# Performance work log

Measured on AMD Instinct MI355X. Metric: run time of the kernel, lower is better.

Reference implementation:

```python
import jax, jax.numpy as jnp
import numpy as np

L, N, E, H = 4096, 1, 1024, 16
DH = E // H
SCALE = DH ** -0.5


def setup_inputs() -> dict:
    key = jax.random.key(0)
    k1, k2, k3 = jax.random.split(key, 3)
    # xavier_uniform-ish scales for faithfulness of magnitude
    lim_qkv = (6.0 / (3 * E + E)) ** 0.5
    lim_out = (6.0 / (E + E)) ** 0.5
    x = jax.random.normal(k1, (L, N, E), dtype=jnp.float32)
    w_qkv = jax.random.uniform(k2, (3 * E, E), dtype=jnp.float32, minval=-lim_qkv, maxval=lim_qkv)
    w_out = jax.random.uniform(k3, (E, E), dtype=jnp.float32, minval=-lim_out, maxval=lim_out)
    return {"x": x, "w_qkv": w_qkv, "w_out": w_out}


def reference(x, w_qkv, w_out):
    # x: [L, N, E]
    qkv = jnp.einsum('lne,fe->lnf', x, w_qkv)          # [L, N, 3E]
    q, k, v = jnp.split(qkv, 3, axis=-1)               # each [L, N, E]

    def to_heads(t):
        # [L, N, E] -> [N*H, L, DH]
        return t.reshape(L, N * H, DH).transpose(1, 0, 2)

    q = to_heads(q) * SCALE
    k = to_heads(k)
    v = to_heads(v)
    attn = jnp.einsum('bld,bmd->blm', q, k)            # [N*H, L, L]
    attn = jax.nn.softmax(attn, axis=-1)
    out = jnp.einsum('blm,bmd->bld', attn, v)          # [N*H, L, DH]
    out = out.transpose(1, 0, 2).reshape(L, N, E)
    return jnp.einsum('lne,fe->lnf', out, w_out)       # [L, N, E]
```

## Files before the change

### kernel.cpp

```cpp
#include <hip/hip_runtime.h>
#include <hip/hip_bf16.h>
#include <stdint.h>

#define L_SEQ 4096
#define EMB   1024
#define NHEAD 16
#define DHEAD 64

#define SM_SCALE 0.18033688011112042f
#define SM_FIXED_MAX 12.0f

typedef __attribute__((ext_vector_type(8))) short short8;
typedef __attribute__((ext_vector_type(4))) short s16x4;
typedef __attribute__((ext_vector_type(4))) float f32x4;
typedef __attribute__((ext_vector_type(2))) unsigned uint2v;

struct Pack8 { f32x4 lo, hi; };

__device__ inline short f2bf(float f) {
  union { float f; unsigned u; } c; c.f = f;
  unsigned r = (c.u + 0x7fffu + ((c.u >> 16) & 1u)) >> 16;
  return (short)(unsigned short)r;
}
__device__ inline unsigned fbits(float f) {
  union { float f; unsigned u; } c; c.f = f; return c.u;
}
__device__ inline unsigned pack_trunc(float f0, float f1) {
#if __has_builtin(__builtin_amdgcn_perm)
  return __builtin_amdgcn_perm(fbits(f1), fbits(f0), 0x07060302u);
#else
  return (fbits(f0) >> 16) | (fbits(f1) & 0xffff0000u);
#endif
}

#if __has_builtin(__builtin_amdgcn_exp2f)
#define EXP2F(x) __builtin_amdgcn_exp2f(x)
#else
#define EXP2F(x) exp2f(x)
#endif

__device__ inline void pl16swap(unsigned &x, unsigned &y) {
#if __has_builtin(__builtin_amdgcn_permlane16_swap)
  auto r = __builtin_amdgcn_permlane16_swap(x, y, false, false);
  x = r[0]; y = r[1];
#else
  asm volatile("v_permlane16_swap_b32 %0, %1" : "+v"(x), "+v"(y));
#endif
}

__device__ inline short8 mk8(unsigned d0, unsigned d1, unsigned d2, unsigned d3) {
  union { unsigned u[4]; short8 s; } c;
  c.u[0] = d0; c.u[1] = d1; c.u[2] = d2; c.u[3] = d3;
  return c.s;
}

template<bool F32>
__device__ inline auto ld8(const void* p, size_t off) {
  if constexpr (F32) {
    const float* f = (const float*)p + off;
    Pack8 r; r.lo = *(const f32x4*)f; r.hi = *(const f32x4*)(f + 4);
    return r;
  } else {
    return *(const short8*)((const short*)p + off);
  }
}
__device__ inline short8 cvt8(Pack8 r) {
  short8 o;
#pragma unroll
  for (int j = 0; j < 4; ++j) { o[j] = f2bf(r.lo[j]); o[4 + j] = f2bf(r.hi[j]); }
  return o;
}
__device__ inline short8 cvt8(short8 r) { return r; }

#define MFMA16(a, b, c) __builtin_amdgcn_mfma_f32_16x16x32_bf16(a, b, c, 0, 0, 0)
#define FZERO ((f32x4){0.f, 0.f, 0.f, 0.f})

__global__ __launch_bounds__(256)
void conv_kernel(const float* __restrict__ in, short* __restrict__ out, int n) {
  int i = (blockIdx.x * 256 + threadIdx.x) * 8;
  if (i >= n) return;
  Pack8 r; r.lo = *(const f32x4*)(in + i); r.hi = *(const f32x4*)(in + i + 4);
  *(short8*)(out + i) = cvt8(r);
}

template<bool AF32, bool BF32, bool CF32>
__global__ __launch_bounds__(256, 2)
void gemm_bt(const void* __restrict__ Av, const void* __restrict__ Bv,
             void* __restrict__ Cv, int N, int K, int lda, int ldc,
             float cscale) {
  __shared__ __align__(16) short At[128 * 40];
  __shared__ __align__(16) short Bt[128 * 40];

  const int tid  = threadIdx.x;
  const int lane = tid & 63;
  const int wave = tid >> 6;
  const int quad = lane >> 4;
  const int l15  = lane & 15;
  const int q8   = quad << 3;

  const int nbn = N >> 7;
  const int bm  = (blockIdx.x / nbn) << 7;
  const int bn  = (blockIdx.x % nbn) << 7;
  const int wr  = wave >> 1;
  const int wc  = wave & 1;

  const int s0 = tid, s1 = tid + 256;
  const int ar0 = s0 >> 2, ac0 = (s0 & 3) << 3;
  const int ar1 = s1 >> 2, ac1 = (s1 & 3) << 3;

  const size_t aoff0 = (size_t)(bm + ar0) * lda + ac0;
  const size_t aoff1 = (size_t)(bm + ar1) * lda + ac1;
  const size_t boff0 = (size_t)(bn + ar0) * K + ac0;
  const size_t boff1 = (size_t)(bn + ar1) * K + ac1;

  f32x4 acc[4][4];
#pragma unroll
  for (int r = 0; r < 4; ++r)
#pragma unroll
    for (int c = 0; c < 4; ++c) acc[r][c] = FZERO;

  auto ga0 = ld8<AF32>(Av, aoff0);
  auto ga1 = ld8<AF32>(Av, aoff1);
  auto gb0 = ld8<BF32>(Bv, boff0);
  auto gb1 = ld8<BF32>(Bv, boff1);

  const int arow = (wr * 64 + l15) * 40 + q8;
  const int brow = (wc * 64 + l15) * 40 + q8;

  const int nk = K >> 5;
  for (int kt = 0; kt < nk; ++kt) {
    __syncthreads();
    *(short8*)(At + ar0 * 40 + ac0) = cvt8(ga0);
    *(short8*)(At + ar1 * 40 + ac1) = cvt8(ga1);
    *(short8*)(Bt + ar0 * 40 + ac0) = cvt8(gb0);
    *(short8*)(Bt + ar1 * 40 + ac1) = cvt8(gb1);
    __syncthreads();

    if (kt + 1 < nk) {
      const size_t k0 = (size_t)(kt + 1) << 5;
      ga0 = ld8<AF32>(Av, aoff0 + k0);
      ga1 = ld8<AF32>(Av, aoff1 + k0);
      gb0 = ld8<BF32>(Bv, boff0 + k0);
      gb1 = ld8<BF32>(Bv, boff1 + k0);
    }

    short8 af[4], bf[4];
#pragma unroll
    for (int r = 0; r < 4; ++r) af[r] = *(const short8*)(At + arow + r * 640);
#pragma unroll
    for (int c = 0; c < 4; ++c) bf[c] = *(const short8*)(Bt + brow + c * 640);
#pragma unroll
    for (int r = 0; r < 4; ++r)
#pragma unroll
      for (int c = 0; c < 4; ++c)
        acc[r][c] = MFMA16(af[r], bf[c], acc[r][c]);
  }

#pragma unroll
  for (int r = 0; r < 4; ++r) {
#pragma unroll
    for (int c = 0; c < 4; ++c) {
      const int col = bn + wc * 64 + c * 16 + l15;
#pragma unroll
      for (int reg = 0; reg < 4; ++reg) {
        const int row = bm + wr * 64 + r * 16 + quad * 4 + reg;
        const float v = acc[r][c][reg] * cscale;
        if constexpr (CF32) ((float*)Cv)[(size_t)row * ldc + col] = v;
        else                ((short*)Cv)[(size_t)row * ldc + col] = f2bf(v);
      }
    }
  }
}

__global__ __launch_bounds__(256, 2)
void gemm_qkv(const short* __restrict__ A, const float* __restrict__ B,
              short* __restrict__ qb, short* __restrict__ kb,
              short* __restrict__ vt) {
  __shared__ __align__(16) short At[128 * 40];
  __shared__ __align__(16) short Bt[128 * 40];

  const int tid  = threadIdx.x;
  const int lane = tid & 63;
  const int wave = tid >> 6;
  const int quad = lane >> 4;
  const int l15  = lane & 15;
  const int q8   = quad << 3;

  const int bm  = (blockIdx.x / 24) << 7;
  const int bn  = (blockIdx.x % 24) << 7;
  const int wr  = wave >> 1;
  const int wc  = wave & 1;

  const int s0 = tid, s1 = tid + 256;
  const int ar0 = s0 >> 2, ac0 = (s0 & 3) << 3;
  const int ar1 = s1 >> 2, ac1 = (s1 & 3) << 3;

  const size_t aoff0 = (size_t)(bm + ar0) * EMB + ac0;
  const size_t aoff1 = (size_t)(bm + ar1) * EMB + ac1;
  const size_t boff0 = (size_t)(bn + ar0) * EMB + ac0;
  const size_t boff1 = (size_t)(bn + ar1) * EMB + ac1;

  f32x4 acc[4][4];
#pragma unroll
  for (int r = 0; r < 4; ++r)
#pragma unroll
    for (int c = 0; c < 4; ++c) acc[r][c] = FZERO;

  short8 ga0 = *(const short8*)(A + aoff0);
  short8 ga1 = *(const short8*)(A + aoff1);
  Pack8  gb0 = ld8<true>(B, boff0);
  Pack8  gb1 = ld8<true>(B, boff1);

  const int arow = (wr * 64 + l15) * 40 + q8;
  const int brow = (wc * 64 + l15) * 40 + q8;

  for (int kt = 0; kt < 32; ++kt) {
    __syncthreads();
    *(short8*)(At + ar0 * 40 + ac0) = ga0;
    *(short8*)(At + ar1 * 40 + ac1) = ga1;
    *(short8*)(Bt + ar0 * 40 + ac0) = cvt8(gb0);
    *(short8*)(Bt + ar1 * 40 + ac1) = cvt8(gb1);
    __syncthreads();

    if (kt + 1 < 32) {
      const size_t k0 = (size_t)(kt + 1) << 5;
      ga0 = *(const short8*)(A + aoff0 + k0);
      ga1 = *(const short8*)(A + aoff1 + k0);
      gb0 = ld8<true>(B, boff0 + k0);
      gb1 = ld8<true>(B, boff1 + k0);
    }

    short8 af[4], bf[4];
#pragma unroll
    for (int r = 0; r < 4; ++r) af[r] = *(const short8*)(At + arow + r * 640);
#pragma unroll
    for (int c = 0; c < 4; ++c) bf[c] = *(const short8*)(Bt + brow + c * 640);
#pragma unroll
    for (int r = 0; r < 4; ++r)
#pragma unroll
      for (int c = 0; c < 4; ++c)
        acc[r][c] = MFMA16(af[r], bf[c], acc[r][c]);
  }

  if (bn < 2048) {
    short* dst = (bn < 1024) ? qb : kb;
    const int bcol = (bn < 1024) ? bn : bn - 1024;
    const float cs = (bn < 1024) ? SM_SCALE : 1.0f;
#pragma unroll
    for (int r = 0; r < 4; ++r)
#pragma unroll
      for (int c = 0; c < 4; ++c) {
        const int col = bcol + wc * 64 + c * 16 + l15;
#pragma unroll
        for (int reg = 0; reg < 4; ++reg) {
          const int row = bm + wr * 64 + r * 16 + quad * 4 + reg;
          dst[(size_t)row * EMB + col] = f2bf(acc[r][c][reg] * cs);
        }
      }
  } else {
    const int bcol = bn - 2048;
#pragma unroll
    for (int r = 0; r < 4; ++r)
#pragma unroll
      for (int c = 0; c < 4; ++c) {
        const int col  = bcol + wc * 64 + c * 16 + l15;
        const int rowb = bm + wr * 64 + r * 16 + quad * 4;
        s16x4 pk;
#pragma unroll
        for (int reg = 0; reg < 4; ++reg) pk[reg] = f2bf(acc[r][c][reg]);
        *(s16x4*)(vt + (size_t)col * L_SEQ + rowb) = pk;
      }
  }
}

__global__ __launch_bounds__(256, 2)
void attn_kernel(short* __restrict__ qo, const short* __restrict__ kbuf,
                 const short* __restrict__ vtbuf) {
  __shared__ __align__(16) short Kt[2][64 * 72];
  __shared__ __align__(16) short Vt[2][64 * 72];

  const int tid  = threadIdx.x;
  const int lane = tid & 63;
  const int w    = tid >> 6;
  const int quad = lane >> 4;
  const int l15  = lane & 15;
  const int q8   = quad << 3;
  const int vb   = ((quad & 1) << 4) | ((quad >> 1) << 3);

  const int h    = blockIdx.x >> 5;
  const int qblk = blockIdx.x & 31;
  const int hcol = h * 64;

  const int srow = tid >> 3;
  const int sc8  = (tid & 7) << 3;

  short8 qf[2][2];
#pragma unroll
  for (int g = 0; g < 2; ++g) {
    const short* qp = qo + (size_t)(qblk * 128 + w * 32 + g * 16 + l15) * EMB + hcol;
    qf[g][0] = *(const short8*)(qp + q8);
    qf[g][1] = *(const short8*)(qp + 32 + q8);
  }

  const short8 vone = {0x3F80, 0x3F80, 0x3F80, 0x3F80,
                       0x3F80, 0x3F80, 0x3F80, 0x3F80};

  f32x4 o[2][4];
#pragma unroll
  for (int g = 0; g < 2; ++g)
#pragma unroll
    for (int f = 0; f < 4; ++f) o[g][f] = FZERO;
  f32x4 l_c[2] = {FZERO, FZERO};

  const size_t koff0 = (size_t)srow * EMB + hcol + sc8;
  const size_t voff0 = (size_t)(hcol + srow) * L_SEQ + sc8;
  const size_t krr = (size_t)32 * EMB;
  const size_t vrr = (size_t)32 * L_SEQ;

  short8 gk0 = *(const short8*)(kbuf + koff0);
  short8 gk1 = *(const short8*)(kbuf + koff0 + krr);
  short8 gv0 = *(const short8*)(vtbuf + voff0);
  short8 gv1 = *(const short8*)(vtbuf + voff0 + vrr);

  for (int t = 0; t < 64; ++t) {
    short* const ktb = &Kt[t & 1][0];
    short* const vtb = &Vt[t & 1][0];

    *(short8*)(ktb + srow * 72 + sc8) = gk0;
    *(short8*)(ktb + (srow + 32) * 72 + sc8) = gk1;
    *(short8*)(vtb + srow * 72 + sc8) = gv0;
    *(short8*)(vtb + (srow + 32) * 72 + sc8) = gv1;
    __syncthreads();

    if (t < 63) {
      const size_t kk = (size_t)(t + 1) * 64;
      gk0 = *(const short8*)(kbuf + koff0 + kk * EMB);
      gk1 = *(const short8*)(kbuf + koff0 + krr + kk * EMB);
      gv0 = *(const short8*)(vtbuf + voff0 + kk);
      gv1 = *(const short8*)(vtbuf + voff0 + vrr + kk);
    }

    f32x4 s[2][4];
#pragma unroll
    for (int f = 0; f < 4; ++f) {
      const int krow = (f * 16 + l15) * 72;
      short8 kf0 = *(const short8*)(ktb + krow + q8);
      short8 kf1 = *(const short8*)(ktb + krow + 32 + q8);
      s[0][f] = MFMA16(kf0, qf[0][0], FZERO);
      s[0][f] = MFMA16(kf1, qf[0][1], s[0][f]);
      s[1][f] = MFMA16(kf0, qf[1][0], FZERO);
      s[1][f] = MFMA16(kf1, qf[1][1], s[1][f]);
    }

    short8 pa[2][2];
#pragma unroll
    for (int g = 0; g < 2; ++g) {
      float p[4][4];
#pragma unroll
      for (int f = 0; f < 4; ++f)
#pragma unroll
        for (int r = 0; r < 4; ++r)
          p[f][r] = EXP2F(s[g][f][r] - SM_FIXED_MAX);

      unsigned pk[4][2];
#pragma unroll
      for (int f = 0; f < 4; ++f) {
        pk[f][0] = pack_trunc(p[f][0], p[f][1]);
        pk[f][1] = pack_trunc(p[f][2], p[f][3]);
      }
      pl16swap(pk[0][0], pk[1][0]);
      pl16swap(pk[0][1], pk[1][1]);
      pl16swap(pk[2][0], pk[3][0]);
      pl16swap(pk[2][1], pk[3][1]);
      pa[g][0] = mk8(pk[0][0], pk[0][1], pk[1][0], pk[1][1]);
      pa[g][1] = mk8(pk[2][0], pk[2][1], pk[3][0], pk[3][1]);

      f32x4 rsv = MFMA16(pa[g][0], vone, FZERO);
      rsv = MFMA16(pa[g][1], vone, rsv);
#pragma unroll
      for (int r = 0; r < 4; ++r) l_c[g][r] += rsv[r];
    }

#pragma unroll
    for (int f = 0; f < 4; ++f) {
      const int vrow = (f * 16 + l15) * 72;
      short8 v0 = *(const short8*)(vtb + vrow + vb);
      short8 v1 = *(const short8*)(vtb + vrow + 32 + vb);
      o[0][f] = MFMA16(pa[0][0], v0, o[0][f]);
      o[0][f] = MFMA16(pa[0][1], v1, o[0][f]);
      o[1][f] = MFMA16(pa[1][0], v0, o[1][f]);
      o[1][f] = MFMA16(pa[1][1], v1, o[1][f]);
    }
  }

  __syncthreads();
  short* const pw = &Kt[0][0] + w * (32 * 72);
#pragma unroll
  for (int g = 0; g < 2; ++g) {
    f32x4 inv;
#pragma unroll
    for (int r = 0; r < 4; ++r) inv[r] = 1.0f / l_c[g][r];
    short* const pg = pw + g * (16 * 72);
#pragma unroll
    for (int f = 0; f < 4; ++f)
#pragma unroll
      for (int r = 0; r < 4; ++r)
        pg[(quad * 4 + r) * 72 + f * 16 + l15] = f2bf(o[g][f][r] * inv[r]);
  }

#pragma unroll
  for (int rr = 0; rr < 4; ++rr) {
    const int row = (lane >> 3) + rr * 8;
    const int c8  = (lane & 7) << 3;
    short8 gv = *(const short8*)(pw + row * 72 + c8);
    *(short8*)(qo + (size_t)(qblk * 128 + w * 32 + row) * EMB + hcol + c8) = gv;
  }
}

extern "C" void kernel_launch(void* const* d_in, const int* in_sizes, int n_in,
                              void* d_out, int out_size, void* d_ws, size_t ws_size,
                              hipStream_t stream) {
  (void)in_sizes; (void)n_in; (void)out_size; (void)ws_size;
  const float* x     = (const float*)d_in[0];
  const float* w_qkv = (const float*)d_in[1];
  const float* w_out = (const float*)d_in[2];

  short* qbuf  = (short*)d_ws;
  short* x_bf  = qbuf + (size_t)L_SEQ * EMB;
  short* wo_bf = x_bf;
  short* kbuf  = (short*)d_out;
  short* vtbuf = kbuf + (size_t)L_SEQ * EMB;
  float* outp  = (float*)d_out;

  conv_kernel<<<dim3(L_SEQ * EMB / 2048), 256, 0, stream>>>(x, x_bf, L_SEQ * EMB);

  gemm_qkv<<<dim3(768), 256, 0, stream>>>(x_bf, w_qkv, qbuf, kbuf, vtbuf);

  conv_kernel<<<dim3(EMB * EMB / 2048), 256, 0, stream>>>(w_out, wo_bf, EMB * EMB);

  attn_kernel<<<dim3(NHEAD * (L_SEQ / 128)), 256, 0, stream>>>(qbuf, kbuf, vtbuf);

  gemm_bt<false, false, true><<<dim3(256), 256, 0, stream>>>(qbuf, wo_bf, outp, EMB, EMB, EMB, EMB, 1.0f);
}
```

Measured before the change: 220.2 us.

## Double attention query tile per block to 256 rows for K/V reuse

Each attention block now handles 256 query rows (64 per wave, four 16-row groups) instead of 128, halving the grid to 256 blocks and halving K/V global loads and LDS staging per query. Shared memory is merged into one buffer, which is reused for the larger output staging area. Launch bounds drop to one block per SM to allow the doubled accumulator and score registers. The risk is lower occupancy and only 256 blocks on a 256-CU device, so there is less latency hiding.

```diff
diff --git a/kernel.cpp b/kernel.cpp
--- a/kernel.cpp
+++ b/kernel.cpp
@@ -273,11 +273,10 @@
   }
 }
 
-__global__ __launch_bounds__(256, 2)
+__global__ __launch_bounds__(256, 1)
 void attn_kernel(short* __restrict__ qo, const short* __restrict__ kbuf,
                  const short* __restrict__ vtbuf) {
-  __shared__ __align__(16) short Kt[2][64 * 72];
-  __shared__ __align__(16) short Vt[2][64 * 72];
+  __shared__ __align__(16) short SH[4 * 64 * 72];
 
   const int tid  = threadIdx.x;
   const int lane = tid & 63;
@@ -287,17 +286,18 @@
   const int q8   = quad << 3;
   const int vb   = ((quad & 1) << 4) | ((quad >> 1) << 3);
 
-  const int h    = blockIdx.x >> 5;
-  const int qblk = blockIdx.x & 31;
+  const int h    = blockIdx.x >> 4;
+  const int qblk = blockIdx.x & 15;
   const int hcol = h * 64;
+  const int qrow0 = qblk * 256 + w * 64;
 
   const int srow = tid >> 3;
   const int sc8  = (tid & 7) << 3;
 
-  short8 qf[2][2];
-#pragma unroll
-  for (int g = 0; g < 2; ++g) {
-    const short* qp = qo + (size_t)(qblk * 128 + w * 32 + g * 16 + l15) * EMB + hcol;
+  short8 qf[4][2];
+#pragma unroll
+  for (int g = 0; g < 4; ++g) {
+    const short* qp = qo + (size_t)(qrow0 + g * 16 + l15) * EMB + hcol;
     qf[g][0] = *(const short8*)(qp + q8);
     qf[g][1] = *(const short8*)(qp + 32 + q8);
   }
@@ -305,12 +305,12 @@
   const short8 vone = {0x3F80, 0x3F80, 0x3F80, 0x3F80,
                        0x3F80, 0x3F80, 0x3F80, 0x3F80};
 
-  f32x4 o[2][4];
-#pragma unroll
-  for (int g = 0; g < 2; ++g)
+  f32x4 o[4][4];
+#pragma unroll
+  for (int g = 0; g < 4; ++g)
 #pragma unroll
     for (int f = 0; f < 4; ++f) o[g][f] = FZERO;
-  f32x4 l_c[2] = {FZERO, FZERO};
+  f32x4 l_c[4] = {FZERO, FZERO, FZERO, FZERO};
 
   const size_t koff0 = (size_t)srow * EMB + hcol + sc8;
   const size_t voff0 = (size_t)(hcol + srow) * L_SEQ + sc8;
@@ -323,8 +323,8 @@
   short8 gv1 = *(const short8*)(vtbuf + voff0 + vrr);
 
   for (int t = 0; t < 64; ++t) {
-    short* const ktb = &Kt[t & 1][0];
-    short* const vtb = &Vt[t & 1][0];
+    short* const ktb = SH + (t & 1) * (64 * 72);
+    short* const vtb = SH + (2 + (t & 1)) * (64 * 72);
 
     *(short8*)(ktb + srow * 72 + sc8) = gk0;
     *(short8*)(ktb + (srow + 32) * 72 + sc8) = gk1;
@@ -340,21 +340,22 @@
       gv1 = *(const short8*)(vtbuf + voff0 + vrr + kk);
     }
 
-    f32x4 s[2][4];
+    f32x4 s[4][4];
 #pragma unroll
     for (int f = 0; f < 4; ++f) {
       const int krow = (f * 16 + l15) * 72;
       short8 kf0 = *(const short8*)(ktb + krow + q8);
       short8 kf1 = *(const short8*)(ktb + krow + 32 + q8);
-      s[0][f] = MFMA16(kf0, qf[0][0], FZERO);
-      s[0][f] = MFMA16(kf1, qf[0][1], s[0][f]);
-      s[1][f] = MFMA16(kf0, qf[1][0], FZERO);
-      s[1][f] = MFMA16(kf1, qf[1][1], s[1][f]);
-    }
-
-    short8 pa[2][2];
-#pragma unroll
-    for (int g = 0; g < 2; ++g) {
+#pragma unroll
+      for (int g = 0; g < 4; ++g) {
+        s[g][f] = MFMA16(kf0, qf[g][0], FZERO);
+        s[g][f] = MFMA16(kf1, qf[g][1], s[g][f]);
+      }
+    }
+
+    short8 pa[4][2];
+#pragma unroll
+    for (int g = 0; g < 4; ++g) {
       float p[4][4];
 #pragma unroll
       for (int f = 0; f < 4; ++f)
@@ -386,17 +387,18 @@
       const int vrow = (f * 16 + l15) * 72;
       short8 v0 = *(const short8*)(vtb + vrow + vb);
       short8 v1 = *(const short8*)(vtb + vrow + 32 + vb);
-      o[0][f] = MFMA16(pa[0][0], v0, o[0][f]);
-      o[0][f] = MFMA16(pa[0][1], v1, o[0][f]);
-      o[1][f] = MFMA16(pa[1][0], v0, o[1][f]);
-      o[1][f] = MFMA16(pa[1][1], v1, o[1][f]);
+#pragma unroll
+      for (int g = 0; g < 4; ++g) {
+        o[g][f] = MFMA16(pa[g][0], v0, o[g][f]);
+        o[g][f] = MFMA16(pa[g][1], v1, o[g][f]);
+      }
     }
   }
 
   __syncthreads();
-  short* const pw = &Kt[0][0] + w * (32 * 72);
-#pragma unroll
-  for (int g = 0; g < 2; ++g) {
+  short* const pw = SH + w * (64 * 72);
+#pragma unroll
+  for (int g = 0; g < 4; ++g) {
     f32x4 inv;
 #pragma unroll
     for (int r = 0; r < 4; ++r) inv[r] = 1.0f / l_c[g][r];
@@ -409,11 +411,11 @@
   }
 
 #pragma unroll
-  for (int rr = 0; rr < 4; ++rr) {
+  for (int rr = 0; rr < 8; ++rr) {
     const int row = (lane >> 3) + rr * 8;
     const int c8  = (lane & 7) << 3;
     short8 gv = *(const short8*)(pw + row * 72 + c8);
-    *(short8*)(qo + (size_t)(qblk * 128 + w * 32 + row) * EMB + hcol + c8) = gv;
+    *(short8*)(qo + (size_t)(qrow0 + row) * EMB + hcol + c8) = gv;
   }
 }
 
@@ -438,7 +440,7 @@
 
   conv_kernel<<<dim3(EMB * EMB / 2048), 256, 0, stream>>>(w_out, wo_bf, EMB * EMB);
 
-  attn_kernel<<<dim3(NHEAD * (L_SEQ / 128)), 256, 0, stream>>>(qbuf, kbuf, vtbuf);
+  attn_kernel<<<dim3(NHEAD * (L_SEQ / 256)), 256, 0, stream>>>(qbuf, kbuf, vtbuf);
 
   gemm_bt<false, false, true><<<dim3(256), 256, 0, stream>>>(qbuf, wo_bf, outp, EMB, EMB, EMB, EMB, 1.0f);
 }
```

Measured after the change: 251.0 us. 1.14x slower.

## Stage GEMM tiles via global_load_lds DMA with double buffering and swizzle

Applied to the files above, without the earlier changes.

Both GEMMs now copy bf16 A (and B in the output projection) straight from global memory into LDS with global_load_lds. The shared tiles are double-buffered with an XOR swizzle in place of padding, which cuts each k-step to one barrier and overlaps the next tile's load with the current MFMAs. The attention kernel also raises wave priority around its MFMA blocks via s_setprio. This roughly doubles LDS use per block, which may limit occupancy, and the swizzled addressing has to match exactly between the writes and the reads.

```diff
diff --git a/kernel.cpp b/kernel.cpp
--- a/kernel.cpp
+++ b/kernel.cpp
@@ -13,7 +13,6 @@
 typedef __attribute__((ext_vector_type(8))) short short8;
 typedef __attribute__((ext_vector_type(4))) short s16x4;
 typedef __attribute__((ext_vector_type(4))) float f32x4;
-typedef __attribute__((ext_vector_type(2))) unsigned uint2v;
 
 struct Pack8 { f32x4 lo, hi; };
 
@@ -75,6 +74,24 @@
 #define MFMA16(a, b, c) __builtin_amdgcn_mfma_f32_16x16x32_bf16(a, b, c, 0, 0, 0)
 #define FZERO ((f32x4){0.f, 0.f, 0.f, 0.f})
 
+__device__ inline void stage16(const void* g, void* l) {
+  __builtin_amdgcn_global_load_lds(
+      (const __attribute__((address_space(1))) void*)g,
+      (__attribute__((address_space(3))) void*)l, 16, 0, 0);
+}
+
+__device__ inline void stage_tile(const short* src, int ld, int k0,
+                                  short* lds, int tid) {
+#pragma unroll
+  for (int j = 0; j < 2; ++j) {
+    const int s = j * 256 + tid;
+    const int row = s >> 2;
+    const int q = (s & 3) ^ ((s >> 3) & 3);
+    stage16(src + (size_t)row * ld + k0 + q * 8,
+            lds + (size_t)(j * 256 + (tid & ~63)) * 8);
+  }
+}
+
 __global__ __launch_bounds__(256)
 void conv_kernel(const float* __restrict__ in, short* __restrict__ out, int n) {
   int i = (blockIdx.x * 256 + threadIdx.x) * 8;
@@ -83,13 +100,82 @@
   *(short8*)(out + i) = cvt8(r);
 }
 
-template<bool AF32, bool BF32, bool CF32>
 __global__ __launch_bounds__(256, 2)
-void gemm_bt(const void* __restrict__ Av, const void* __restrict__ Bv,
-             void* __restrict__ Cv, int N, int K, int lda, int ldc,
-             float cscale) {
-  __shared__ __align__(16) short At[128 * 40];
-  __shared__ __align__(16) short Bt[128 * 40];
+void gemm_bt_dma(const short* __restrict__ A, const short* __restrict__ B,
+                 float* __restrict__ C, int N, int K) {
+  __shared__ __align__(16) short At[2][128 * 32];
+  __shared__ __align__(16) short Bt[2][128 * 32];
+
+  const int tid  = threadIdx.x;
+  const int lane = tid & 63;
+  const int wave = tid >> 6;
+  const int quad = lane >> 4;
+  const int l15  = lane & 15;
+
+  const int nbn = N >> 7;
+  const int bm  = (blockIdx.x / nbn) << 7;
+  const int bn  = (blockIdx.x % nbn) << 7;
+  const int wr  = wave >> 1;
+  const int wc  = wave & 1;
+
+  const short* Ab = A + (size_t)bm * K;
+  const short* Bb = B + (size_t)bn * K;
+
+  f32x4 acc[4][4];
+#pragma unroll
+  for (int r = 0; r < 4; ++r)
+#pragma unroll
+    for (int c = 0; c < 4; ++c) acc[r][c] = FZERO;
+
+  stage_tile(Ab, K, 0, At[0], tid);
+  stage_tile(Bb, K, 0, Bt[0], tid);
+  __syncthreads();
+
+  const int swz  = (quad ^ ((l15 >> 1) & 3)) << 3;
+  const int arow = (wr * 64 + l15) * 32 + swz;
+  const int brow = (wc * 64 + l15) * 32 + swz;
+
+  int buf = 0;
+  const int nk = K >> 5;
+  for (int kt = 0; kt < nk; ++kt) {
+    if (kt + 1 < nk) {
+      stage_tile(Ab, K, (kt + 1) << 5, At[buf ^ 1], tid);
+      stage_tile(Bb, K, (kt + 1) << 5, Bt[buf ^ 1], tid);
+    }
+    short8 af[4], bf[4];
+#pragma unroll
+    for (int r = 0; r < 4; ++r) af[r] = *(const short8*)(At[buf] + arow + r * 512);
+#pragma unroll
+    for (int c = 0; c < 4; ++c) bf[c] = *(const short8*)(Bt[buf] + brow + c * 512);
+#pragma unroll
+    for (int r = 0; r < 4; ++r)
+#pragma unroll
+      for (int c = 0; c < 4; ++c)
+        acc[r][c] = MFMA16(af[r], bf[c], acc[r][c]);
+    __syncthreads();
+    buf ^= 1;
+  }
+
+#pragma unroll
+  for (int r = 0; r < 4; ++r) {
+#pragma unroll
+    for (int c = 0; c < 4; ++c) {
+      const int col = bn + wc * 64 + c * 16 + l15;
+#pragma unroll
+      for (int reg = 0; reg < 4; ++reg) {
+        const int row = bm + wr * 64 + r * 16 + quad * 4 + reg;
+        C[(size_t)row * N + col] = acc[r][c][reg];
+      }
+    }
+  }
+}
+
+__global__ __launch_bounds__(256, 2)
+void gemm_qkv(const short* __restrict__ A, const float* __restrict__ B,
+              short* __restrict__ qb, short* __restrict__ kb,
+              short* __restrict__ vt) {
+  __shared__ __align__(16) short At[2][128 * 32];
+  __shared__ __align__(16) short Bt[2][128 * 40];
 
   const int tid  = threadIdx.x;
   const int lane = tid & 63;
@@ -98,107 +184,15 @@
   const int l15  = lane & 15;
   const int q8   = quad << 3;
 
-  const int nbn = N >> 7;
-  const int bm  = (blockIdx.x / nbn) << 7;
-  const int bn  = (blockIdx.x % nbn) << 7;
-  const int wr  = wave >> 1;
-  const int wc  = wave & 1;
-
-  const int s0 = tid, s1 = tid + 256;
-  const int ar0 = s0 >> 2, ac0 = (s0 & 3) << 3;
-  const int ar1 = s1 >> 2, ac1 = (s1 & 3) << 3;
-
-  const size_t aoff0 = (size_t)(bm + ar0) * lda + ac0;
-  const size_t aoff1 = (size_t)(bm + ar1) * lda + ac1;
-  const size_t boff0 = (size_t)(bn + ar0) * K + ac0;
-  const size_t boff1 = (size_t)(bn + ar1) * K + ac1;
-
-  f32x4 acc[4][4];
-#pragma unroll
-  for (int r = 0; r < 4; ++r)
-#pragma unroll
-    for (int c = 0; c < 4; ++c) acc[r][c] = FZERO;
-
-  auto ga0 = ld8<AF32>(Av, aoff0);
-  auto ga1 = ld8<AF32>(Av, aoff1);
-  auto gb0 = ld8<BF32>(Bv, boff0);
-  auto gb1 = ld8<BF32>(Bv, boff1);
-
-  const int arow = (wr * 64 + l15) * 40 + q8;
-  const int brow = (wc * 64 + l15) * 40 + q8;
-
-  const int nk = K >> 5;
-  for (int kt = 0; kt < nk; ++kt) {
-    __syncthreads();
-    *(short8*)(At + ar0 * 40 + ac0) = cvt8(ga0);
-    *(short8*)(At + ar1 * 40 + ac1) = cvt8(ga1);
-    *(short8*)(Bt + ar0 * 40 + ac0) = cvt8(gb0);
-    *(short8*)(Bt + ar1 * 40 + ac1) = cvt8(gb1);
-    __syncthreads();
-
-    if (kt + 1 < nk) {
-      const size_t k0 = (size_t)(kt + 1) << 5;
-      ga0 = ld8<AF32>(Av, aoff0 + k0);
-      ga1 = ld8<AF32>(Av, aoff1 + k0);
-      gb0 = ld8<BF32>(Bv, boff0 + k0);
-      gb1 = ld8<BF32>(Bv, boff1 + k0);
-    }
-
-    short8 af[4], bf[4];
-#pragma unroll
-    for (int r = 0; r < 4; ++r) af[r] = *(const short8*)(At + arow + r * 640);
-#pragma unroll
-    for (int c = 0; c < 4; ++c) bf[c] = *(const short8*)(Bt + brow + c * 640);
-#pragma unroll
-    for (int r = 0; r < 4; ++r)
-#pragma unroll
-      for (int c = 0; c < 4; ++c)
-        acc[r][c] = MFMA16(af[r], bf[c], acc[r][c]);
-  }
-
-#pragma unroll
-  for (int r = 0; r < 4; ++r) {
-#pragma unroll
-    for (int c = 0; c < 4; ++c) {
-      const int col = bn + wc * 64 + c * 16 + l15;
-#pragma unroll
-      for (int reg = 0; reg < 4; ++reg) {
-        const int row = bm + wr * 64 + r * 16 + quad * 4 + reg;
-        const float v = acc[r][c][reg] * cscale;
-        if constexpr (CF32) ((float*)Cv)[(size_t)row * ldc + col] = v;
-        else                ((short*)Cv)[(size_t)row * ldc + col] = f2bf(v);
-      }
-    }
-  }
-}
-
-__global__ __launch_bounds__(256, 2)
-void gemm_qkv(const short* __restrict__ A, const float* __restrict__ B,
-              short* __restrict__ qb, short* __restrict__ kb,
-              short* __restrict__ vt) {
-  __shared__ __align__(16) short At[128 * 40];
-  __shared__ __align__(16) short Bt[128 * 40];
-
-  const int tid  = threadIdx.x;
-  const int lane = tid & 63;
-  const int wave = tid >> 6;
-  const int quad = lane >> 4;
-  const int l15  = lane & 15;
-  const int q8   = quad << 3;
-
   const int bm  = (blockIdx.x / 24) << 7;
   const int bn  = (blockIdx.x % 24) << 7;
   const int wr  = wave >> 1;
   const int wc  = wave & 1;
 
-  const int s0 = tid, s1 = tid + 256;
-  const int ar0 = s0 >> 2, ac0 = (s0 & 3) << 3;
-  const int ar1 = s1 >> 2, ac1 = (s1 & 3) << 3;
-
-  const size_t aoff0 = (size_t)(bm + ar0) * EMB + ac0;
-  const size_t aoff1 = (size_t)(bm + ar1) * EMB + ac1;
-  const size_t boff0 = (size_t)(bn + ar0) * EMB + ac0;
-  const size_t boff1 = (size_t)(bn + ar1) * EMB + ac1;
+  const short* Ab = A + (size_t)bm * EMB;
+  const int br0 = tid >> 2, bc0 = (tid & 3) << 3;
+  const size_t boff0 = (size_t)(bn + br0) * EMB + bc0;
+  const size_t boff1 = (size_t)(bn + 64 + br0) * EMB + bc0;
 
   f32x4 acc[4][4];
 #pragma unroll
@@ -206,40 +200,41 @@
 #pragma unroll
     for (int c = 0; c < 4; ++c) acc[r][c] = FZERO;
 
-  short8 ga0 = *(const short8*)(A + aoff0);
-  short8 ga1 = *(const short8*)(A + aoff1);
-  Pack8  gb0 = ld8<true>(B, boff0);
-  Pack8  gb1 = ld8<true>(B, boff1);
-
-  const int arow = (wr * 64 + l15) * 40 + q8;
+  stage_tile(Ab, EMB, 0, At[0], tid);
+  Pack8 gb0 = ld8<true>(B, boff0);
+  Pack8 gb1 = ld8<true>(B, boff1);
+  *(short8*)(Bt[0] + br0 * 40 + bc0) = cvt8(gb0);
+  *(short8*)(Bt[0] + (64 + br0) * 40 + bc0) = cvt8(gb1);
+  gb0 = ld8<true>(B, boff0 + 32);
+  gb1 = ld8<true>(B, boff1 + 32);
+  __syncthreads();
+
+  const int arow = (wr * 64 + l15) * 32 + ((quad ^ ((l15 >> 1) & 3)) << 3);
   const int brow = (wc * 64 + l15) * 40 + q8;
 
+  int buf = 0;
   for (int kt = 0; kt < 32; ++kt) {
-    __syncthreads();
-    *(short8*)(At + ar0 * 40 + ac0) = ga0;
-    *(short8*)(At + ar1 * 40 + ac1) = ga1;
-    *(short8*)(Bt + ar0 * 40 + ac0) = cvt8(gb0);
-    *(short8*)(Bt + ar1 * 40 + ac1) = cvt8(gb1);
-    __syncthreads();
-
     if (kt + 1 < 32) {
-      const size_t k0 = (size_t)(kt + 1) << 5;
-      ga0 = *(const short8*)(A + aoff0 + k0);
-      ga1 = *(const short8*)(A + aoff1 + k0);
-      gb0 = ld8<true>(B, boff0 + k0);
-      gb1 = ld8<true>(B, boff1 + k0);
-    }
-
+      stage_tile(Ab, EMB, (kt + 1) << 5, At[buf ^ 1], tid);
+      *(short8*)(Bt[buf ^ 1] + br0 * 40 + bc0) = cvt8(gb0);
+      *(short8*)(Bt[buf ^ 1] + (64 + br0) * 40 + bc0) = cvt8(gb1);
+      if (kt + 2 < 32) {
+        gb0 = ld8<true>(B, boff0 + (size_t)(kt + 2) * 32);
+        gb1 = ld8<true>(B, boff1 + (size_t)(kt + 2) * 32);
+      }
+    }
     short8 af[4], bf[4];
 #pragma unroll
-    for (int r = 0; r < 4; ++r) af[r] = *(const short8*)(At + arow + r * 640);
-#pragma unroll
-    for (int c = 0; c < 4; ++c) bf[c] = *(const short8*)(Bt + brow + c * 640);
+    for (int r = 0; r < 4; ++r) af[r] = *(const short8*)(At[buf] + arow + r * 512);
+#pragma unroll
+    for (int c = 0; c < 4; ++c) bf[c] = *(const short8*)(Bt[buf] + brow + c * 640);
 #pragma unroll
     for (int r = 0; r < 4; ++r)
 #pragma unroll
       for (int c = 0; c < 4; ++c)
         acc[r][c] = MFMA16(af[r], bf[c], acc[r][c]);
+    __syncthreads();
+    buf ^= 1;
   }
 
   if (bn < 2048) {
@@ -341,6 +336,7 @@
     }
 
     f32x4 s[2][4];
+    __builtin_amdgcn_s_setprio(1);
 #pragma unroll
     for (int f = 0; f < 4; ++f) {
       const int krow = (f * 16 + l15) * 72;
@@ -351,6 +347,7 @@
       s[1][f] = MFMA16(kf0, qf[1][0], FZERO);
       s[1][f] = MFMA16(kf1, qf[1][1], s[1][f]);
     }
+    __builtin_amdgcn_s_setprio(0);
 
     short8 pa[2][2];
 #pragma unroll
@@ -381,6 +378,7 @@
       for (int r = 0; r < 4; ++r) l_c[g][r] += rsv[r];
     }
 
+    __builtin_amdgcn_s_setprio(1);
 #pragma unroll
     for (int f = 0; f < 4; ++f) {
       const int vrow = (f * 16 + l15) * 72;
@@ -391,6 +389,7 @@
       o[1][f] = MFMA16(pa[1][0], v0, o[1][f]);
       o[1][f] = MFMA16(pa[1][1], v1, o[1][f]);
     }
+    __builtin_amdgcn_s_setprio(0);
   }
 
   __syncthreads();
@@ -440,5 +439,5 @@
 
   attn_kernel<<<dim3(NHEAD * (L_SEQ / 128)), 256, 0, stream>>>(qbuf, kbuf, vtbuf);
 
-  gemm_bt<false, false, true><<<dim3(256), 256, 0, stream>>>(qbuf, wo_bf, outp, EMB, EMB, EMB, EMB, 1.0f);
-}
+  gemm_bt_dma<<<dim3(256), 256, 0, stream>>>(qbuf, wo_bf, outp, EMB, EMB);
+}
```

New measurement: 226.2 us. +2.8%, slower.

## Fuse w_out bf16 conversion into a narrower output GEMM with more blocks

Applied to the files above, without the earlier changes.

Drops the separate conversion kernel for w_out and replaces the generic gemm_bt with a dedicated gemm_out. gemm_out loads fp32 weights and converts them to bf16 while staging them into shared memory. It uses 128x64 tiles, giving 512 blocks instead of 256 to better fill the GPU. It also raises gemm_qkv's launch_bounds occupancy hint from 2 to 3, which may force register spilling. Because the weights are now converted inside each block, every block re-converts its slice of w_out, adding some redundant conversion work.

```diff
diff --git a/kernel.cpp b/kernel.cpp
--- a/kernel.cpp
+++ b/kernel.cpp
@@ -13,7 +13,6 @@
 typedef __attribute__((ext_vector_type(8))) short short8;
 typedef __attribute__((ext_vector_type(4))) short s16x4;
 typedef __attribute__((ext_vector_type(4))) float f32x4;
-typedef __attribute__((ext_vector_type(2))) unsigned uint2v;
 
 struct Pack8 { f32x4 lo, hi; };
 
@@ -83,96 +82,7 @@
   *(short8*)(out + i) = cvt8(r);
 }
 
-template<bool AF32, bool BF32, bool CF32>
-__global__ __launch_bounds__(256, 2)
-void gemm_bt(const void* __restrict__ Av, const void* __restrict__ Bv,
-             void* __restrict__ Cv, int N, int K, int lda, int ldc,
-             float cscale) {
-  __shared__ __align__(16) short At[128 * 40];
-  __shared__ __align__(16) short Bt[128 * 40];
-
-  const int tid  = threadIdx.x;
-  const int lane = tid & 63;
-  const int wave = tid >> 6;
-  const int quad = lane >> 4;
-  const int l15  = lane & 15;
-  const int q8   = quad << 3;
-
-  const int nbn = N >> 7;
-  const int bm  = (blockIdx.x / nbn) << 7;
-  const int bn  = (blockIdx.x % nbn) << 7;
-  const int wr  = wave >> 1;
-  const int wc  = wave & 1;
-
-  const int s0 = tid, s1 = tid + 256;
-  const int ar0 = s0 >> 2, ac0 = (s0 & 3) << 3;
-  const int ar1 = s1 >> 2, ac1 = (s1 & 3) << 3;
-
-  const size_t aoff0 = (size_t)(bm + ar0) * lda + ac0;
-  const size_t aoff1 = (size_t)(bm + ar1) * lda + ac1;
-  const size_t boff0 = (size_t)(bn + ar0) * K + ac0;
-  const size_t boff1 = (size_t)(bn + ar1) * K + ac1;
-
-  f32x4 acc[4][4];
-#pragma unroll
-  for (int r = 0; r < 4; ++r)
-#pragma unroll
-    for (int c = 0; c < 4; ++c) acc[r][c] = FZERO;
-
-  auto ga0 = ld8<AF32>(Av, aoff0);
-  auto ga1 = ld8<AF32>(Av, aoff1);
-  auto gb0 = ld8<BF32>(Bv, boff0);
-  auto gb1 = ld8<BF32>(Bv, boff1);
-
-  const int arow = (wr * 64 + l15) * 40 + q8;
-  const int brow = (wc * 64 + l15) * 40 + q8;
-
-  const int nk = K >> 5;
-  for (int kt = 0; kt < nk; ++kt) {
-    __syncthreads();
-    *(short8*)(At + ar0 * 40 + ac0) = cvt8(ga0);
-    *(short8*)(At + ar1 * 40 + ac1) = cvt8(ga1);
-    *(short8*)(Bt + ar0 * 40 + ac0) = cvt8(gb0);
-    *(short8*)(Bt + ar1 * 40 + ac1) = cvt8(gb1);
-    __syncthreads();
-
-    if (kt + 1 < nk) {
-      const size_t k0 = (size_t)(kt + 1) << 5;
-      ga0 = ld8<AF32>(Av, aoff0 + k0);
-      ga1 = ld8<AF32>(Av, aoff1 + k0);
-      gb0 = ld8<BF32>(Bv, boff0 + k0);
-      gb1 = ld8<BF32>(Bv, boff1 + k0);
-    }
-
-    short8 af[4], bf[4];
-#pragma unroll
-    for (int r = 0; r < 4; ++r) af[r] = *(const short8*)(At + arow + r * 640);
-#pragma unroll
-    for (int c = 0; c < 4; ++c) bf[c] = *(const short8*)(Bt + brow + c * 640);
-#pragma unroll
-    for (int r = 0; r < 4; ++r)
-#pragma unroll
-      for (int c = 0; c < 4; ++c)
-        acc[r][c] = MFMA16(af[r], bf[c], acc[r][c]);
-  }
-
-#pragma unroll
-  for (int r = 0; r < 4; ++r) {
-#pragma unroll
-    for (int c = 0; c < 4; ++c) {
-      const int col = bn + wc * 64 + c * 16 + l15;
-#pragma unroll
-      for (int reg = 0; reg < 4; ++reg) {
-        const int row = bm + wr * 64 + r * 16 + quad * 4 + reg;
-        const float v = acc[r][c][reg] * cscale;
-        if constexpr (CF32) ((float*)Cv)[(size_t)row * ldc + col] = v;
-        else                ((short*)Cv)[(size_t)row * ldc + col] = f2bf(v);
-      }
-    }
-  }
-}
-
-__global__ __launch_bounds__(256, 2)
+__global__ __launch_bounds__(256, 3)
 void gemm_qkv(const short* __restrict__ A, const float* __restrict__ B,
               short* __restrict__ qb, short* __restrict__ kb,
               short* __restrict__ vt) {
@@ -270,6 +180,86 @@
         for (int reg = 0; reg < 4; ++reg) pk[reg] = f2bf(acc[r][c][reg]);
         *(s16x4*)(vt + (size_t)col * L_SEQ + rowb) = pk;
       }
+  }
+}
+
+__global__ __launch_bounds__(256, 2)
+void gemm_out(const short* __restrict__ A, const float* __restrict__ B,
+              float* __restrict__ C) {
+  __shared__ __align__(16) short At[128 * 40];
+  __shared__ __align__(16) short Bt[64 * 40];
+
+  const int tid  = threadIdx.x;
+  const int lane = tid & 63;
+  const int wave = tid >> 6;
+  const int quad = lane >> 4;
+  const int l15  = lane & 15;
+  const int q8   = quad << 3;
+
+  const int bm  = (blockIdx.x >> 4) << 7;
+  const int bn  = (blockIdx.x & 15) << 6;
+  const int wr  = wave >> 1;
+  const int wc  = wave & 1;
+
+  const int s0 = tid, s1 = tid + 256;
+  const int ar0 = s0 >> 2, ac0 = (s0 & 3) << 3;
+  const int ar1 = s1 >> 2, ac1 = (s1 & 3) << 3;
+  const int br0 = tid >> 2, bc0 = (tid & 3) << 3;
+
+  const size_t aoff0 = (size_t)(bm + ar0) * EMB + ac0;
+  const size_t aoff1 = (size_t)(bm + ar1) * EMB + ac1;
+  const size_t boff0 = (size_t)(bn + br0) * EMB + bc0;
+
+  f32x4 acc[4][2];
+#pragma unroll
+  for (int r = 0; r < 4; ++r)
+#pragma unroll
+    for (int c = 0; c < 2; ++c) acc[r][c] = FZERO;
+
+  short8 ga0 = *(const short8*)(A + aoff0);
+  short8 ga1 = *(const short8*)(A + aoff1);
+  Pack8  gb0 = ld8<true>(B, boff0);
+
+  const int arow = (wr * 64 + l15) * 40 + q8;
+  const int brow = (wc * 32 + l15) * 40 + q8;
+
+  for (int kt = 0; kt < 32; ++kt) {
+    __syncthreads();
+    *(short8*)(At + ar0 * 40 + ac0) = ga0;
+    *(short8*)(At + ar1 * 40 + ac1) = ga1;
+    *(short8*)(Bt + br0 * 40 + bc0) = cvt8(gb0);
+    __syncthreads();
+
+    if (kt + 1 < 32) {
+      const size_t k0 = (size_t)(kt + 1) << 5;
+      ga0 = *(const short8*)(A + aoff0 + k0);
+      ga1 = *(const short8*)(A + aoff1 + k0);
+      gb0 = ld8<true>(B, boff0 + k0);
+    }
+
+    short8 af[4], bf[2];
+#pragma unroll
+    for (int r = 0; r < 4; ++r) af[r] = *(const short8*)(At + arow + r * 640);
+#pragma unroll
+    for (int c = 0; c < 2; ++c) bf[c] = *(const short8*)(Bt + brow + c * 640);
+#pragma unroll
+    for (int r = 0; r < 4; ++r)
+#pragma unroll
+      for (int c = 0; c < 2; ++c)
+        acc[r][c] = MFMA16(af[r], bf[c], acc[r][c]);
+  }
+
+#pragma unroll
+  for (int r = 0; r < 4; ++r) {
+#pragma unroll
+    for (int c = 0; c < 2; ++c) {
+      const int col = bn + wc * 32 + c * 16 + l15;
+#pragma unroll
+      for (int reg = 0; reg < 4; ++reg) {
+        const int row = bm + wr * 64 + r * 16 + quad * 4 + reg;
+        C[(size_t)row * EMB + col] = acc[r][c][reg];
+      }
+    }
   }
 }
 
@@ -427,7 +417,6 @@
 
   short* qbuf  = (short*)d_ws;
   short* x_bf  = qbuf + (size_t)L_SEQ * EMB;
-  short* wo_bf = x_bf;
   short* kbuf  = (short*)d_out;
   short* vtbuf = kbuf + (size_t)L_SEQ * EMB;
   float* outp  = (float*)d_out;
@@ -436,9 +425,7 @@
 
   gemm_qkv<<<dim3(768), 256, 0, stream>>>(x_bf, w_qkv, qbuf, kbuf, vtbuf);
 
-  conv_kernel<<<dim3(EMB * EMB / 2048), 256, 0, stream>>>(w_out, wo_bf, EMB * EMB);
-
   attn_kernel<<<dim3(NHEAD * (L_SEQ / 128)), 256, 0, stream>>>(qbuf, kbuf, vtbuf);
 
-  gemm_bt<false, false, true><<<dim3(256), 256, 0, stream>>>(qbuf, wo_bf, outp, EMB, EMB, EMB, EMB, 1.0f);
-}
+  gemm_out<<<dim3(512), 256, 0, stream>>>(qbuf, w_out, outp);
+}
```

New measurement: 222.6 us. Within noise of the previous version (+1.1%).
